# Kernel optimization log

Measured on AMD Instinct MI355X. Metric: run time of the kernel, lower is better.

Reference implementation:

```python
import jax, jax.numpy as jnp
import numpy as np

FS = 30.0          # sampling frequency (Hz)
HIGH_PASS = 40.0   # BPM
LOW_PASS = 250.0   # BPM


def _band_idx(delta_t):
    # static band-pass bin selection (mirrors CalculateNormPSD)
    F = delta_t // 2 + 1
    freqs = np.linspace(0.0, FS / 2.0, F)
    mask = (freqs >= HIGH_PASS / 60.0) & (freqs <= LOW_PASS / 60.0)
    return np.nonzero(mask)[0]


def setup_inputs() -> dict:
    key = jax.random.key(0)
    k1, k2 = jax.random.split(key)
    B, M, T, K, DT = 2, 2048, 4096, 16, 150
    model_output = jax.random.normal(k1, (B, M, T), dtype=jnp.float32)
    offsets = jax.random.randint(k2, (B, M, K), 0, T - DT + 1)
    return {"model_output": model_output, "offsets": offsets, "delta_t": DT}


def reference(model_output, offsets, delta_t):
    B, M, T = model_output.shape
    K = offsets.shape[-1]
    # gather K random segments of length delta_t per (video, location)
    idx = offsets[..., None] + jnp.arange(delta_t)                    # (B,M,K,dt)
    src = jnp.broadcast_to(model_output[:, :, None, :], (B, M, K, T))
    segs = jnp.take_along_axis(src, idx, axis=-1)                     # (B,M,K,dt)
    # normalized PSD (CalculateNormPSD, zero_pad=0)
    segs = segs - jnp.mean(segs, axis=-1, keepdims=True)
    X = jnp.fft.rfft(segs, axis=-1) / delta_t                         # norm='forward'
    psd = X.real ** 2 + X.imag ** 2                                   # (B,M,K,F)
    band = _band_idx(delta_t)
    psd = psd[..., band]
    psd = psd / jnp.sum(psd, axis=-1, keepdims=True)                  # (B,M,K,Fb)
    Fb = psd.shape[-1]
    N = M * K
    S = psd.reshape(B, N, Fb)
    A, Bm = S[0], S[1]

    def pair_sum(P, Q):
        # sum_{i,j} mean_f (P_i - Q_j)^2, closed form
        t = (Q.shape[0] * jnp.sum(P ** 2) + P.shape[0] * jnp.sum(Q ** 2)
             - 2.0 * jnp.dot(jnp.sum(P, axis=0), jnp.sum(Q, axis=0)))
        return t / Fb

    # exclude_same: diagonal (i==j) terms are exactly zero, so they drop out
    self_a = pair_sum(A, A) / (N * (N - 1))
    self_b = pair_sum(Bm, Bm) / (N * (N - 1))
    pos_loss_1 = (self_a + self_b) / 2.0
    pos_loss_2 = pair_sum(A, Bm) / (N * N)
    return pos_loss_1 + pos_loss_2
```

## Files before the change

### kernel.cpp

```cpp
#include <hip/hip_runtime.h>
#include <stdint.h>


#define T_LEN 4096
#define KSEG 16
#define NROWS 4096
#define DTLEN 150
#define NBIN 17
#define SEG_STRIDE 156

typedef float v2f __attribute__((ext_vector_type(2)));

__device__ __constant__ float C2TAB[18] = {
  1.9719921f, 1.9562952f, 1.9371663f, 1.9146390f, 1.8887527f, 1.8595530f,
  1.8270909f, 1.7914235f, 1.7526134f, 1.7107286f, 1.6658425f, 1.6180340f,
  1.5673869f, 1.5139901f, 1.4579372f, 1.3993267f, 1.3382612f, 1.2748480f
};

__device__ __forceinline__ void gload_lds16(const float* g, float* l) {
  __builtin_amdgcn_global_load_lds(
      (const __attribute__((address_space(1))) void*)g,
      (__attribute__((address_space(3))) void*)l,
      16, 0, 0);
}

__global__ __launch_bounds__(64) void psd_partials(const float* __restrict__ mo,
                                                   const int* __restrict__ offs,
                                                   float* __restrict__ ws) {
  __shared__ float tile[KSEG * SEG_STRIDE];

  const int r = blockIdx.x;
  const int t = threadIdx.x;
  const int seg = t >> 2;
  const int g = t & 3;

  const int off = offs[r * KSEG + seg];
  const float* __restrict__ rowp = mo + (size_t)r * T_LEN;

  #pragma unroll
  for (int s = 0; s < KSEG; ++s) {
    const int off_s = __shfl(off, s << 2, 64);
    const int al = off_s & ~3;
    const int bound = 37 + ((off_s & 3) == 3);
    if (t <= bound)
      gload_lds16(rowp + al + 4 * t, &tile[s * SEG_STRIDE]);
  }
  __syncthreads();

  const int boff = (g == 0) ? 0 : (1 + 4 * g);
  const v2f c01 = {C2TAB[boff], C2TAB[boff + 1]};
  const v2f c23 = {C2TAB[boff + 2], C2TAB[boff + 3]};
  const float c4 = C2TAB[boff + 4];

  v2f a01 = {0.f, 0.f}, a23 = {0.f, 0.f}, b01 = {0.f, 0.f}, b23 = {0.f, 0.f};
  float a4 = 0.f, b4 = 0.f;

  const float* __restrict__ x = &tile[seg * SEG_STRIDE + (off & 3)];
  #pragma unroll 5
  for (int n = 0; n < DTLEN; n += 2) {
    const float x0 = x[n];
    const float x1 = x[n + 1];
    const v2f x0v = {x0, x0};
    const v2f x1v = {x1, x1};
    b01 = __builtin_elementwise_fma(c01, a01, x0v - b01);
    b23 = __builtin_elementwise_fma(c23, a23, x0v - b23);
    b4  = fmaf(c4, a4, x0 - b4);
    a01 = __builtin_elementwise_fma(c01, b01, x1v - a01);
    a23 = __builtin_elementwise_fma(c23, b23, x1v - a23);
    a4  = fmaf(c4, b4, x1 - a4);
  }

  const v2f p01 = __builtin_elementwise_fma(a01, a01, b01 * b01) - c01 * (a01 * b01);
  const v2f p23 = __builtin_elementwise_fma(a23, a23, b23 * b23) - c23 * (a23 * b23);
  float p[5];
  p[0] = p01.x; p[1] = p01.y; p[2] = p23.x; p[3] = p23.y;
  p[4] = (g == 0) ? (fmaf(a4, a4, b4 * b4) - c4 * a4 * b4) : 0.0f;

  float bs = p[0] + p[1] + p[2] + p[3] + p[4];
  bs += __shfl_xor(bs, 1, 64);
  bs += __shfl_xor(bs, 2, 64);
  const float inv = 1.0f / bs;
  #pragma unroll
  for (int j = 0; j < 5; ++j) p[j] *= inv;

  float ssq = p[0]*p[0] + p[1]*p[1] + p[2]*p[2] + p[3]*p[3] + p[4]*p[4];
  #pragma unroll
  for (int m = 1; m <= 32; m <<= 1) ssq += __shfl_xor(ssq, m, 64);

  #pragma unroll
  for (int m = 4; m <= 32; m <<= 1) {
    #pragma unroll
    for (int j = 0; j < 5; ++j) p[j] += __shfl_xor(p[j], m, 64);
  }

  if (t == 0) ws[r] = ssq;
  if (t < 4) {
    const int nb = (t == 0) ? 5 : 4;
    #pragma unroll
    for (int j = 0; j < 5; ++j)
      if (j < nb) ws[(1 + boff + j) * NROWS + r] = p[j];
  }
}

__global__ __launch_bounds__(1024) void reduce_final(const float* __restrict__ ws,
                                                     float* __restrict__ out) {
  __shared__ double fin[36];
  const int t = threadIdx.x;
  const int w = t >> 6, lane = t & 63;

  for (int p = w; p < 36; p += 16) {
    const float4* __restrict__ base =
        (const float4*)(ws + (p >> 1) * NROWS + (p & 1) * 2048);
    double a = 0.0;
    #pragma unroll
    for (int q = 0; q < 8; ++q) {
      float4 f = base[lane + 64 * q];
      a += (double)f.x + (double)f.y + (double)f.z + (double)f.w;
    }
    #pragma unroll
    for (int m = 32; m >= 1; m >>= 1) a += __shfl_xor(a, m, 64);
    if (lane == 0) fin[p] = a;
  }
  __syncthreads();

  if (t == 0) {
    double sumA2 = fin[0], sumB2 = fin[1];
    double dAA = 0.0, dBB = 0.0, dAB = 0.0;
    #pragma unroll
    for (int f = 0; f < NBIN; ++f) {
      double ca = fin[2 * (1 + f)];
      double cb = fin[2 * (1 + f) + 1];
      dAA += ca * ca;
      dBB += cb * cb;
      dAB += ca * cb;
    }
    const double N = 32768.0;
    const double invFb   = 1.0 / 17.0;
    const double invNN1  = 1.0 / (32768.0 * 32767.0);
    const double invNN   = 1.0 / (32768.0 * 32768.0);
    double pAA = (2.0 * N * sumA2 - 2.0 * dAA) * invFb;
    double pBB = (2.0 * N * sumB2 - 2.0 * dBB) * invFb;
    double pAB = (N * sumA2 + N * sumB2 - 2.0 * dAB) * invFb;
    double selfa = pAA * invNN1;
    double selfb = pBB * invNN1;
    out[0] = (float)(0.5 * (selfa + selfb) + pAB * invNN);
  }
}

extern "C" void kernel_launch(void* const* d_in, const int* in_sizes, int n_in,
                              void* d_out, int out_size, void* d_ws, size_t ws_size,
                              hipStream_t stream) {
  const float* mo = (const float*)d_in[0];
  const int* offs = (const int*)d_in[1];
  float* out = (float*)d_out;
  float* ws = (float*)d_ws;

  psd_partials<<<NROWS, 64, 0, stream>>>(mo, offs, ws);
  reduce_final<<<1, 1024, 0, stream>>>(ws, out);
}
```

Measured before the change: 21.79 us.

## Load full rows into LDS, process two rows per block, pre-reduce partials

Each block now handles two rows, one per wavefront. Every wave copies its entire 4096-float row into LDS with coalesced 16-byte global-to-LDS loads, replacing the earlier per-segment aligned loads. Per-row partial sums are combined in shared memory before being written, which halves the workspace the final reduction kernel has to read. The trade-off is that whole rows are fetched even though only the sampled segments are needed, so total global traffic and LDS use per block go up.

```diff
diff --git a/kernel.cpp b/kernel.cpp
--- a/kernel.cpp
+++ b/kernel.cpp
@@ -3,11 +3,10 @@
 
 
 #define T_LEN 4096
-#define KSEG 16
 #define NROWS 4096
 #define DTLEN 150
 #define NBIN 17
-#define SEG_STRIDE 156
+#define NBLK 2048
 
 typedef float v2f __attribute__((ext_vector_type(2)));
 
@@ -24,29 +23,29 @@
       16, 0, 0);
 }
 
-__global__ __launch_bounds__(64) void psd_partials(const float* __restrict__ mo,
-                                                   const int* __restrict__ offs,
-                                                   float* __restrict__ ws) {
-  __shared__ float tile[KSEG * SEG_STRIDE];
+__global__ __launch_bounds__(128) void psd_partials(const float* __restrict__ mo,
+                                                    const int* __restrict__ offs,
+                                                    float* __restrict__ ws) {
+  __shared__ float tile[2 * T_LEN];
+  __shared__ float sm[2][18];
 
-  const int r = blockIdx.x;
+  const int b = blockIdx.x;
   const int t = threadIdx.x;
-  const int seg = t >> 2;
-  const int g = t & 3;
+  const int w = t >> 6;
+  const int lane = t & 63;
+  const int r = (b << 1) + w;
 
-  const int off = offs[r * KSEG + seg];
-  const float* __restrict__ rowp = mo + (size_t)r * T_LEN;
+  const float* __restrict__ rowp = mo + ((size_t)r << 12);
+  float* trow = &tile[w << 12];
 
   #pragma unroll
-  for (int s = 0; s < KSEG; ++s) {
-    const int off_s = __shfl(off, s << 2, 64);
-    const int al = off_s & ~3;
-    const int bound = 37 + ((off_s & 3) == 3);
-    if (t <= bound)
-      gload_lds16(rowp + al + 4 * t, &tile[s * SEG_STRIDE]);
-  }
+  for (int i = 0; i < 16; ++i)
+    gload_lds16(rowp + (i << 8) + (lane << 2), trow + (i << 8));
   __syncthreads();
 
+  const int seg = lane >> 2;
+  const int g = lane & 3;
+  const int off = offs[(r << 4) + seg];
   const int boff = (g == 0) ? 0 : (1 + 4 * g);
   const v2f c01 = {C2TAB[boff], C2TAB[boff + 1]};
   const v2f c23 = {C2TAB[boff + 2], C2TAB[boff + 3]};
@@ -55,7 +54,7 @@
   v2f a01 = {0.f, 0.f}, a23 = {0.f, 0.f}, b01 = {0.f, 0.f}, b23 = {0.f, 0.f};
   float a4 = 0.f, b4 = 0.f;
 
-  const float* __restrict__ x = &tile[seg * SEG_STRIDE + (off & 3)];
+  const float* __restrict__ x = trow + off;
   #pragma unroll 5
   for (int n = 0; n < DTLEN; n += 2) {
     const float x0 = x[n];
@@ -93,13 +92,16 @@
     for (int j = 0; j < 5; ++j) p[j] += __shfl_xor(p[j], m, 64);
   }
 
-  if (t == 0) ws[r] = ssq;
-  if (t < 4) {
-    const int nb = (t == 0) ? 5 : 4;
+  if (lane == 0) sm[w][0] = ssq;
+  if (lane < 4) {
+    const int nb = (lane == 0) ? 5 : 4;
     #pragma unroll
     for (int j = 0; j < 5; ++j)
-      if (j < nb) ws[(1 + boff + j) * NROWS + r] = p[j];
+      if (j < nb) sm[w][1 + boff + j] = p[j];
   }
+  __syncthreads();
+
+  if (t < 18) ws[(t << 11) + b] = sm[0][t] + sm[1][t];
 }
 
 __global__ __launch_bounds__(1024) void reduce_final(const float* __restrict__ ws,
@@ -110,11 +112,11 @@
 
   for (int p = w; p < 36; p += 16) {
     const float4* __restrict__ base =
-        (const float4*)(ws + (p >> 1) * NROWS + (p & 1) * 2048);
+        (const float4*)(ws + ((p >> 1) << 11) + ((p & 1) << 10));
     double a = 0.0;
     #pragma unroll
-    for (int q = 0; q < 8; ++q) {
-      float4 f = base[lane + 64 * q];
+    for (int q = 0; q < 4; ++q) {
+      float4 f = base[lane + (q << 6)];
       a += (double)f.x + (double)f.y + (double)f.z + (double)f.w;
     }
     #pragma unroll
@@ -135,9 +137,9 @@
       dAB += ca * cb;
     }
     const double N = 32768.0;
-    const double invFb   = 1.0 / 17.0;
-    const double invNN1  = 1.0 / (32768.0 * 32767.0);
-    const double invNN   = 1.0 / (32768.0 * 32768.0);
+    const double invFb  = 1.0 / 17.0;
+    const double invNN1 = 1.0 / (32768.0 * 32767.0);
+    const double invNN  = 1.0 / (32768.0 * 32768.0);
     double pAA = (2.0 * N * sumA2 - 2.0 * dAA) * invFb;
     double pBB = (2.0 * N * sumB2 - 2.0 * dBB) * invFb;
     double pAB = (N * sumA2 + N * sumB2 - 2.0 * dAB) * invFb;
@@ -155,6 +157,6 @@
   float* out = (float*)d_out;
   float* ws = (float*)d_ws;
 
-  psd_partials<<<NROWS, 64, 0, stream>>>(mo, offs, ws);
+  psd_partials<<<NBLK, 128, 0, stream>>>(mo, offs, ws);
   reduce_final<<<1, 1024, 0, stream>>>(ws, out);
 }
```

Result: slower. 26.92 us (+23.6%).
